# Optimization experiments

Hardware: AMD Instinct MI355X
Metric: run time of the kernel (lower is better)

The kernel has to match this reference:

```python
import jax, jax.numpy as jnp
import numpy as np

NUM_BLOCKS = 3
NUM_CLUSTER = [16, 32, 64]


def _conv(x, w, b):
    # 1x1 conv2d + ReLU (BN folded to identity, eval-mode default stats): x [B,d,N], w [o,d], b [o]
    return jax.nn.relu(jnp.einsum('bdn,od->bon', x, w) + b[None, :, None])


def _segment_pool(feat, idx, nc):
    # Faithful single-pass version of pooling_block: per-cluster max over N,
    # rebroadcast to every node of that cluster. feat [B,d,N], idx [B,N] int.
    B, d, N = feat.shape
    seg = (idx + jnp.arange(B, dtype=idx.dtype)[:, None] * nc).reshape(-1)  # [B*N]
    flat = feat.transpose(0, 2, 1).reshape(B * N, d)
    mx = jax.ops.segment_max(flat, seg, num_segments=B * nc)  # [B*nc, d]
    return mx[seg].reshape(B, N, d).transpose(0, 2, 1)  # [B,d,N]


def setup_inputs() -> dict:
    key = jax.random.key(0)
    ks = jax.random.split(key, 16)
    B, N, K = 8, 16384, 28
    s = 0.05
    f32 = jnp.float32
    return {
        'x': jax.random.normal(ks[0], (B, N, K), f32),
        'clusters': jax.random.randint(ks[1], (NUM_BLOCKS, B, N), 0, min(NUM_CLUSTER), dtype=jnp.int32),
        'w_in': jax.random.normal(ks[2], (256, K), f32) * s,
        'b_in': jnp.zeros((256,), f32),
        'w1': jax.random.normal(ks[3], (NUM_BLOCKS, 64, 256), f32) * s,
        'b1': jnp.zeros((NUM_BLOCKS, 64), f32),
        'w2': jax.random.normal(ks[4], (NUM_BLOCKS, 128, 64), f32) * s,
        'b2': jnp.zeros((NUM_BLOCKS, 128), f32),
        'w3': jax.random.normal(ks[5], (NUM_BLOCKS, 128, 128), f32) * s,
        'b3': jnp.zeros((NUM_BLOCKS, 128), f32),
        'w_out1': jax.random.normal(ks[6], (128, 256), f32) * s,
        'b_out1': jnp.zeros((128,), f32),
        'w_out2': jax.random.normal(ks[7], (128, 128), f32) * s,
        'b_out2': jnp.zeros((128,), f32),
    }


def reference(x, clusters, w_in, b_in, w1, b1, w2, b2, w3, b3, w_out1, b_out1, w_out2, b_out2):
    # mlp_in: conv2d kernel [1,28] contracts the feature width -> [B,256,N]
    f = jax.nn.relu(jnp.einsum('bnk,ok->bon', x, w_in) + b_in[None, :, None])
    for i in range(NUM_BLOCKS):
        f = _conv(f, w1[i], b1[i])          # [B,64,N]
        f = _conv(f, w2[i], b2[i])          # [B,128,N]
        pool = _segment_pool(f, clusters[i], NUM_CLUSTER[i])  # [B,128,N]
        f3 = _conv(f, w3[i], b3[i])         # [B,128,N]
        f = jnp.concatenate([f3, pool], axis=1)  # [B,256,N]
    o1 = _conv(f, w_out1, b_out1)           # [B,128,N]
    o2 = _conv(o1, w_out2, b_out2)          # [B,128,N]
    out_max = o2.max(axis=2)                # global max pool over N
    B, d = out_max.shape
    return out_max.reshape(B, d, 1, 1)
```

## Files before the change

kernel.cpp:

```cpp
#include <hip/hip_runtime.h>


typedef __attribute__((ext_vector_type(8))) short bf16x8;
typedef __attribute__((ext_vector_type(4))) float f32x4;
typedef __attribute__((ext_vector_type(4))) unsigned u32x4;
typedef __attribute__((ext_vector_type(4))) float f32x4v;

#define MFMA16(a, b, c) __builtin_amdgcn_mfma_f32_16x16x32_bf16((a), (b), (c), 0, 0, 0)

#define TPB 512
#define PT 64
#define NPTS 131072
#define NC 16
#define TILES 4
#define NBLK 512

#define FSB 136
#define ASB 72
#define XSB 40

#define U_F256 0
#define U_W1_0 16
#define U_W2_0 48
#define U_W3_0 64
#define U_W1_1 96
#define U_W2_1 112
#define U_W3_1 128
#define U_W1_2 160
#define U_W2_2 176
#define U_W3_2 192
#define U_O1   224
#define U_O2   256
#define N_UNITS 288

__device__ __forceinline__ f32x4 relu4(f32x4 a) {
#pragma unroll
  for (int r = 0; r < 4; ++r) a[r] = fmaxf(a[r], 0.f);
  return a;
}

__device__ __forceinline__ bf16x8 afrag(const short* plane, int stride, int mt, int ks) {
  const int lane = threadIdx.x & 63;
  return *reinterpret_cast<const bf16x8*>(
      plane + (mt * 16 + (lane & 15)) * stride + ks * 32 + (lane >> 4) * 8);
}

__device__ __forceinline__ void bfrag(const unsigned* __restrict__ arena, int unit,
                                      bf16x8& h, bf16x8& l) {
  const bf16x8* p = reinterpret_cast<const bf16x8*>(
      arena + ((size_t)unit * 64 + (threadIdx.x & 63)) * 8);
  h = p[0];
  l = p[1];
}

__device__ __forceinline__ void store_planes(short* hp, short* lp, int stride,
                                             int mt, int n, f32x4 d) {
  const int m0 = mt * 16 + ((threadIdx.x & 63) >> 4) * 4;
#pragma unroll
  for (int r = 0; r < 4; ++r) {
    unsigned uv = __float_as_uint(d[r]);
    unsigned hm = uv & 0xFFFF0000u;
    float lo = d[r] - __uint_as_float(hm);
    hp[(m0 + r) * stride + n] = (short)(hm >> 16);
    lp[(m0 + r) * stride + n] = (short)(__float_as_uint(lo) >> 16);
  }
}

__device__ __forceinline__ void stage_f3(const unsigned* __restrict__ f3g, int tile0,
                                         short* Fhi, short* Flo, int tid) {
  const u32x4* src = reinterpret_cast<const u32x4*>(f3g + (size_t)tile0 * 128);
#pragma unroll
  for (int rr = 0; rr < 4; ++rr) {
    const int idx = rr * TPB + tid;
    const u32x4 p = __builtin_nontemporal_load(src + idx);
    const int pt = idx >> 5, c4 = (idx & 31) * 4;
    uint2 hd, ld;
    hd.x = (p.y & 0xFFFF0000u) | (p.x >> 16);
    hd.y = (p.w & 0xFFFF0000u) | (p.z >> 16);
    ld.x = (p.y << 16) | (p.x & 0xFFFFu);
    ld.y = (p.w << 16) | (p.z & 0xFFFFu);
    *reinterpret_cast<uint2*>(&Fhi[pt * FSB + c4]) = hd;
    *reinterpret_cast<uint2*>(&Flo[pt * FSB + c4]) = ld;
  }
}

__device__ __forceinline__ void write_f3(unsigned* __restrict__ f3g, int tile0,
                                         const short* Fhi, const short* Flo, int tid) {
  u32x4* dst = reinterpret_cast<u32x4*>(f3g + (size_t)tile0 * 128);
#pragma unroll
  for (int rr = 0; rr < 4; ++rr) {
    const int idx = rr * TPB + tid;
    const int pt = idx >> 5, c4 = (idx & 31) * 4;
    const uint2 hd = *reinterpret_cast<const uint2*>(&Fhi[pt * FSB + c4]);
    const uint2 ld = *reinterpret_cast<const uint2*>(&Flo[pt * FSB + c4]);
    u32x4 p;
    p.x = (hd.x << 16) | (ld.x & 0xFFFFu);
    p.y = (hd.x & 0xFFFF0000u) | (ld.x >> 16);
    p.z = (hd.y << 16) | (ld.y & 0xFFFFu);
    p.w = (hd.y & 0xFFFF0000u) | (ld.y >> 16);
    __builtin_nontemporal_store(p, dst + idx);
  }
}

__global__ void __launch_bounds__(64) prep_frags(
    const float* __restrict__ w_in, const float* __restrict__ w1,
    const float* __restrict__ w2, const float* __restrict__ w3,
    const float* __restrict__ wo1, const float* __restrict__ wo2,
    unsigned* __restrict__ arena) {
  const int unit = blockIdx.x;
  const int lane = threadIdx.x;
  const float* W; int KS, Klog, rs, u;
  if (unit < U_W1_0)      { W = w_in;                   u = unit - U_F256; KS = 1; Klog = 28;  rs = 28;  }
  else if (unit < U_W2_0) { W = w1;                     u = unit - U_W1_0; KS = 8; Klog = 256; rs = 256; }
  else if (unit < U_W3_0) { W = w2;                     u = unit - U_W2_0; KS = 2; Klog = 64;  rs = 64;  }
  else if (unit < U_W1_1) { W = w3;                     u = unit - U_W3_0; KS = 4; Klog = 128; rs = 128; }
  else if (unit < U_W2_1) { W = w1 + 64 * 256;          u = unit - U_W1_1; KS = 4; Klog = 128; rs = 256; }
  else if (unit < U_W3_1) { W = w2 + 128 * 64;          u = unit - U_W2_1; KS = 2; Klog = 64;  rs = 64;  }
  else if (unit < U_W1_2) { W = w3 + 128 * 128;         u = unit - U_W3_1; KS = 4; Klog = 128; rs = 128; }
  else if (unit < U_W2_2) { W = w1 + 2 * 64 * 256;      u = unit - U_W1_2; KS = 4; Klog = 128; rs = 256; }
  else if (unit < U_W3_2) { W = w2 + 2 * 128 * 64;      u = unit - U_W2_2; KS = 2; Klog = 64;  rs = 64;  }
  else if (unit < U_O1)   { W = w3 + 2 * 128 * 128;     u = unit - U_W3_2; KS = 4; Klog = 128; rs = 128; }
  else if (unit < U_O2)   { W = wo1;                    u = unit - U_O1;   KS = 4; Klog = 128; rs = 256; }
  else                    { W = wo2;                    u = unit - U_O2;   KS = 4; Klog = 128; rs = 128; }
  const int nt = u / KS, ks = u % KS;
  const int n = nt * 16 + (lane & 15);
  const int k0 = ks * 32 + (lane >> 4) * 8;
  unsigned hiD[4], loD[4];
#pragma unroll
  for (int d = 0; d < 4; ++d) {
    unsigned hu[2], lu[2];
#pragma unroll
    for (int e = 0; e < 2; ++e) {
      const int k = k0 + d * 2 + e;
      float v = (k < Klog) ? W[(size_t)n * rs + k] : 0.f;
      unsigned uv = __float_as_uint(v);
      unsigned hm = uv & 0xFFFF0000u;
      float lo = v - __uint_as_float(hm);
      hu[e] = hm >> 16;
      lu[e] = __float_as_uint(lo) >> 16;
    }
    hiD[d] = hu[0] | (hu[1] << 16);
    loD[d] = lu[0] | (lu[1] << 16);
  }
  unsigned* dst = arena + ((size_t)unit * 64 + lane) * 8;
  *reinterpret_cast<uint4*>(dst)     = make_uint4(hiD[0], hiD[1], hiD[2], hiD[3]);
  *reinterpret_cast<uint4*>(dst + 4) = make_uint4(loD[0], loD[1], loD[2], loD[3]);
}

template<int O>
__global__ void __launch_bounds__(1024) pool_reduce_kern(
    const unsigned* __restrict__ part, const float* __restrict__ W,
    const float* __restrict__ bias, float* __restrict__ poolc_g) {
  __shared__ float pfL[2048];
  __shared__ float Wl[O * 129];
  const int tid = threadIdx.x;
  const int b = blockIdx.x;
  for (int i = tid; i < 2048; i += 1024) pfL[i] = __uint_as_float(part[b * 2048 + i]);
  for (int i = tid; i < O * 128; i += 1024) {
    const int o = i >> 7, k = i & 127;
    Wl[o * 129 + k] = W[o * 256 + 128 + k];
  }
  __syncthreads();
  constexpr int SH = (O == 64) ? 6 : 7;
  for (int e = tid; e < O * 16; e += 1024) {
    const int o = e & (O - 1);
    const int cl = e >> SH;
    float s = bias[o];
    const float* wr = &Wl[o * 129];
    const float* pr = &pfL[cl];
#pragma unroll 4
    for (int k = 0; k < 128; ++k) s = fmaf(wr[k], pr[k * 16], s);
    poolc_g[(size_t)b * (O * 16) + o * 16 + cl] = s;
  }
}

__global__ void __launch_bounds__(TPB, 4) k0_kern(
    const float* __restrict__ x, const int* __restrict__ cls,
    const float* __restrict__ b_in, const float* __restrict__ b1,
    const float* __restrict__ b2, const float* __restrict__ b3,
    const unsigned* __restrict__ arena,
    unsigned* __restrict__ f3g, unsigned* __restrict__ part0) {
  __shared__ short Fhi[PT * FSB], Flo[PT * FSB];
  __shared__ short XA[PT * ASB * 2];
  __shared__ unsigned pool_s[128 * NC];
  short* Xhi = XA;  short* Xlo = XA + PT * XSB;
  short* Ahi = XA;  short* Alo = XA + PT * ASB;
  const int tid = threadIdx.x;
  const int lane = tid & 63, w = tid >> 6, l15 = lane & 15, quad = lane >> 4;
  const int b = blockIdx.x >> 6;
  const int Nt1 = w & 3, mh = w >> 2;
  for (int i = tid; i < 128 * NC; i += TPB) pool_s[i] = 0u;

  float biH[2];
#pragma unroll
  for (int c = 0; c < 2; ++c) biH[c] = b_in[c * 128 + w * 16 + l15];
  const float b1H = b1[Nt1 * 16 + l15];
  const float b2H = b2[w * 16 + l15];
  const float b3H = b3[w * 16 + l15];
  const int n1 = Nt1 * 16 + l15;
  const int n2 = w * 16 + l15;
  const int xpt = (tid < 448) ? tid / 7 : 0;
  const int xc4 = (tid < 448) ? (tid - xpt * 7) * 4 : 0;

  for (int t = 0; t < TILES; ++t) {
    const int tile0 = (blockIdx.x * TILES + t) * PT;
    if (tid < 448) {
      const f32x4v v = __builtin_nontemporal_load(
          reinterpret_cast<const f32x4v*>(x + (size_t)(tile0 + xpt) * 28 + xc4));
      unsigned h0 = __float_as_uint(v.x) & 0xFFFF0000u, h1 = __float_as_uint(v.y) & 0xFFFF0000u;
      unsigned h2 = __float_as_uint(v.z) & 0xFFFF0000u, h3 = __float_as_uint(v.w) & 0xFFFF0000u;
      uint2 hd, ld;
      hd.x = (h0 >> 16) | h1;
      hd.y = (h2 >> 16) | h3;
      ld.x = (__float_as_uint(v.x - __uint_as_float(h0)) >> 16) |
             (__float_as_uint(v.y - __uint_as_float(h1)) & 0xFFFF0000u);
      ld.y = (__float_as_uint(v.z - __uint_as_float(h2)) >> 16) |
             (__float_as_uint(v.w - __uint_as_float(h3)) & 0xFFFF0000u);
      *reinterpret_cast<uint2*>(&Xhi[xpt * XSB + xc4]) = hd;
      *reinterpret_cast<uint2*>(&Xlo[xpt * XSB + xc4]) = ld;
    } else {
      const int p = tid - 448;
      *reinterpret_cast<uint2*>(&Xhi[p * XSB + 28]) = make_uint2(0u, 0u);
      *reinterpret_cast<uint2*>(&Xlo[p * XSB + 28]) = make_uint2(0u, 0u);
    }
    int clP[4][4];
#pragma unroll
    for (int Mt = 0; Mt < 4; ++Mt) {
      int4 v = *reinterpret_cast<const int4*>(cls + tile0 + Mt * 16 + quad * 4);
      clP[Mt][0] = v.x; clP[Mt][1] = v.y; clP[Mt][2] = v.z; clP[Mt][3] = v.w;
    }
    __syncthreads();
    f32x4 a1[2];
#pragma unroll
    for (int m = 0; m < 2; ++m) a1[m] = {b1H, b1H, b1H, b1H};
#pragma unroll 1
    for (int c = 0; c < 2; ++c) {
      f32x4 f6[4];
#pragma unroll
      for (int Mt = 0; Mt < 4; ++Mt) f6[Mt] = {biH[c], biH[c], biH[c], biH[c]};
      {
        bf16x8 bh, bl;
        bfrag(arena, U_F256 + c * 8 + w, bh, bl);
#pragma unroll
        for (int Mt = 0; Mt < 4; ++Mt) {
          const bf16x8 xah = afrag(Xhi, XSB, Mt, 0), xal = afrag(Xlo, XSB, Mt, 0);
          f6[Mt] = MFMA16(xal, bh, MFMA16(xah, bl, MFMA16(xah, bh, f6[Mt])));
        }
      }
#pragma unroll
      for (int Mt = 0; Mt < 4; ++Mt)
        store_planes(Fhi, Flo, FSB, Mt, n2, relu4(f6[Mt]));
      __syncthreads();
#pragma unroll
      for (int ks = 0; ks < 4; ++ks) {
        bf16x8 bh, bl;
        bfrag(arena, U_W1_0 + Nt1 * 8 + c * 4 + ks, bh, bl);
#pragma unroll
        for (int m = 0; m < 2; ++m) {
          const bf16x8 ah = afrag(Fhi, FSB, mh * 2 + m, ks), al = afrag(Flo, FSB, mh * 2 + m, ks);
          a1[m] = MFMA16(al, bh, MFMA16(ah, bl, MFMA16(ah, bh, a1[m])));
        }
      }
      if (c == 1) {
#pragma unroll
        for (int m = 0; m < 2; ++m)
          store_planes(Ahi, Alo, ASB, mh * 2 + m, n1, relu4(a1[m]));
      }
      __syncthreads();
    }
    f32x4 f2[4];
#pragma unroll
    for (int Mt = 0; Mt < 4; ++Mt) f2[Mt] = {b2H, b2H, b2H, b2H};
#pragma unroll
    for (int ks = 0; ks < 2; ++ks) {
      bf16x8 bh, bl;
      bfrag(arena, U_W2_0 + w * 2 + ks, bh, bl);
#pragma unroll
      for (int Mt = 0; Mt < 4; ++Mt) {
        const bf16x8 ah = afrag(Ahi, ASB, Mt, ks), al = afrag(Alo, ASB, Mt, ks);
        f2[Mt] = MFMA16(al, bh, MFMA16(ah, bl, MFMA16(ah, bh, f2[Mt])));
      }
    }
#pragma unroll
    for (int Mt = 0; Mt < 4; ++Mt) {
      f32x4 d = relu4(f2[Mt]);
#pragma unroll
      for (int r = 0; r < 4; ++r)
        atomicMax(&pool_s[n2 * NC + clP[Mt][r]], __float_as_uint(d[r]));
      store_planes(Fhi, Flo, FSB, Mt, n2, d);
    }
    __syncthreads();
    f32x4 f3a[4];
#pragma unroll
    for (int Mt = 0; Mt < 4; ++Mt) f3a[Mt] = {b3H, b3H, b3H, b3H};
#pragma unroll
    for (int ks = 0; ks < 4; ++ks) {
      bf16x8 bh, bl;
      bfrag(arena, U_W3_0 + w * 4 + ks, bh, bl);
#pragma unroll
      for (int Mt = 0; Mt < 4; ++Mt) {
        const bf16x8 ah = afrag(Fhi, FSB, Mt, ks), al = afrag(Flo, FSB, Mt, ks);
        f3a[Mt] = MFMA16(al, bh, MFMA16(ah, bl, MFMA16(ah, bh, f3a[Mt])));
      }
    }
    __syncthreads();
#pragma unroll
    for (int Mt = 0; Mt < 4; ++Mt)
      store_planes(Fhi, Flo, FSB, Mt, n2, relu4(f3a[Mt]));
    __syncthreads();
    write_f3(f3g, tile0, Fhi, Flo, tid);
  }
  for (int i = tid; i < 128 * NC; i += TPB)
    atomicMax(&part0[(size_t)b * 2048 + i], pool_s[i]);
}

__global__ void __launch_bounds__(TPB, 4) kmid_kern(
    unsigned* __restrict__ f3g, const unsigned* __restrict__ arena,
    const float* __restrict__ poolc_g, unsigned* __restrict__ part_cur,
    const int* __restrict__ clg, const int* __restrict__ clp,
    const float* __restrict__ b2s, const float* __restrict__ b3s,
    int uW1, int uW2, int uW3) {
  __shared__ short Fhi[PT * FSB], Flo[PT * FSB];
  __shared__ short Ahi[PT * ASB], Alo[PT * ASB];
  __shared__ unsigned pool_s[128 * NC];
  const int tid = threadIdx.x;
  const int lane = tid & 63, w = tid >> 6, l15 = lane & 15, quad = lane >> 4;
  const int b = blockIdx.x >> 6;
  const int Nt1 = w & 3, mh = w >> 2;
  for (int i = tid; i < 128 * NC; i += TPB) pool_s[i] = 0u;
  const float b2H = b2s[w * 16 + l15];
  const float b3H = b3s[w * 16 + l15];
  const int n1 = Nt1 * 16 + l15;
  const int n2 = w * 16 + l15;

  for (int t = 0; t < TILES; ++t) {
    const int tile0 = (blockIdx.x * TILES + t) * PT;
    stage_f3(f3g, tile0, Fhi, Flo, tid);
    int clG[2][4], clP[4][4];
#pragma unroll
    for (int m = 0; m < 2; ++m) {
      int4 v = *reinterpret_cast<const int4*>(clg + tile0 + (mh * 2 + m) * 16 + quad * 4);
      clG[m][0] = v.x; clG[m][1] = v.y; clG[m][2] = v.z; clG[m][3] = v.w;
    }
#pragma unroll
    for (int Mt = 0; Mt < 4; ++Mt) {
      int4 v = *reinterpret_cast<const int4*>(clp + tile0 + Mt * 16 + quad * 4);
      clP[Mt][0] = v.x; clP[Mt][1] = v.y; clP[Mt][2] = v.z; clP[Mt][3] = v.w;
    }
    __syncthreads();
    f32x4 a1[2];
#pragma unroll
    for (int m = 0; m < 2; ++m)
#pragma unroll
      for (int r = 0; r < 4; ++r)
        a1[m][r] = poolc_g[(size_t)b * 1024 + n1 * 16 + clG[m][r]];
#pragma unroll
    for (int ks = 0; ks < 4; ++ks) {
      bf16x8 bh, bl;
      bfrag(arena, uW1 + Nt1 * 4 + ks, bh, bl);
#pragma unroll
      for (int m = 0; m < 2; ++m) {
        const bf16x8 ah = afrag(Fhi, FSB, mh * 2 + m, ks), al = afrag(Flo, FSB, mh * 2 + m, ks);
        a1[m] = MFMA16(al, bh, MFMA16(ah, bl, MFMA16(ah, bh, a1[m])));
      }
    }
#pragma unroll
    for (int m = 0; m < 2; ++m)
      store_planes(Ahi, Alo, ASB, mh * 2 + m, n1, relu4(a1[m]));
    __syncthreads();
    f32x4 f2[4];
#pragma unroll
    for (int Mt = 0; Mt < 4; ++Mt) f2[Mt] = {b2H, b2H, b2H, b2H};
#pragma unroll
    for (int ks = 0; ks < 2; ++ks) {
      bf16x8 bh, bl;
      bfrag(arena, uW2 + w * 2 + ks, bh, bl);
#pragma unroll
      for (int Mt = 0; Mt < 4; ++Mt) {
        const bf16x8 ah = afrag(Ahi, ASB, Mt, ks), al = afrag(Alo, ASB, Mt, ks);
        f2[Mt] = MFMA16(al, bh, MFMA16(ah, bl, MFMA16(ah, bh, f2[Mt])));
      }
    }
#pragma unroll
    for (int Mt = 0; Mt < 4; ++Mt) {
      f32x4 d = relu4(f2[Mt]);
#pragma unroll
      for (int r = 0; r < 4; ++r)
        atomicMax(&pool_s[n2 * NC + clP[Mt][r]], __float_as_uint(d[r]));
      store_planes(Fhi, Flo, FSB, Mt, n2, d);
    }
    __syncthreads();
    f32x4 f3a[4];
#pragma unroll
    for (int Mt = 0; Mt < 4; ++Mt) f3a[Mt] = {b3H, b3H, b3H, b3H};
#pragma unroll
    for (int ks = 0; ks < 4; ++ks) {
      bf16x8 bh, bl;
      bfrag(arena, uW3 + w * 4 + ks, bh, bl);
#pragma unroll
      for (int Mt = 0; Mt < 4; ++Mt) {
        const bf16x8 ah = afrag(Fhi, FSB, Mt, ks), al = afrag(Flo, FSB, Mt, ks);
        f3a[Mt] = MFMA16(al, bh, MFMA16(ah, bl, MFMA16(ah, bh, f3a[Mt])));
      }
    }
    __syncthreads();
#pragma unroll
    for (int Mt = 0; Mt < 4; ++Mt)
      store_planes(Fhi, Flo, FSB, Mt, n2, relu4(f3a[Mt]));
    __syncthreads();
    write_f3(f3g, tile0, Fhi, Flo, tid);
    __syncthreads();
  }
  for (int i = tid; i < 128 * NC; i += TPB)
    atomicMax(&part_cur[(size_t)b * 2048 + i], pool_s[i]);
}

__global__ void __launch_bounds__(TPB, 4) k3_kern(
    const unsigned* __restrict__ f3g, const unsigned* __restrict__ arena,
    const float* __restrict__ poolco_g, const int* __restrict__ clg,
    const float* __restrict__ bo2, unsigned* __restrict__ out) {
  __shared__ short Fhi[PT * FSB], Flo[PT * FSB];
  const int tid = threadIdx.x;
  const int lane = tid & 63, w = tid >> 6, l15 = lane & 15, quad = lane >> 4;
  const int b = blockIdx.x >> 6;
  const float bo2H = bo2[w * 16 + l15];
  const int n2 = w * 16 + l15;
  float omax = 0.f;

  for (int t = 0; t < TILES; ++t) {
    const int tile0 = (blockIdx.x * TILES + t) * PT;
    stage_f3(f3g, tile0, Fhi, Flo, tid);
    int clA[4][4];
#pragma unroll
    for (int Mt = 0; Mt < 4; ++Mt) {
      int4 v = *reinterpret_cast<const int4*>(clg + tile0 + Mt * 16 + quad * 4);
      clA[Mt][0] = v.x; clA[Mt][1] = v.y; clA[Mt][2] = v.z; clA[Mt][3] = v.w;
    }
    __syncthreads();
    f32x4 o1a[4];
#pragma unroll
    for (int Mt = 0; Mt < 4; ++Mt)
#pragma unroll
      for (int r = 0; r < 4; ++r)
        o1a[Mt][r] = poolco_g[(size_t)b * 2048 + n2 * 16 + clA[Mt][r]];
#pragma unroll
    for (int ks = 0; ks < 4; ++ks) {
      bf16x8 bh, bl;
      bfrag(arena, U_O1 + w * 4 + ks, bh, bl);
#pragma unroll
      for (int Mt = 0; Mt < 4; ++Mt) {
        const bf16x8 ah = afrag(Fhi, FSB, Mt, ks), al = afrag(Flo, FSB, Mt, ks);
        o1a[Mt] = MFMA16(al, bh, MFMA16(ah, bl, MFMA16(ah, bh, o1a[Mt])));
      }
    }
    __syncthreads();
#pragma unroll
    for (int Mt = 0; Mt < 4; ++Mt)
      store_planes(Fhi, Flo, FSB, Mt, n2, relu4(o1a[Mt]));
    __syncthreads();
    f32x4 o2a[4];
#pragma unroll
    for (int Mt = 0; Mt < 4; ++Mt) o2a[Mt] = {bo2H, bo2H, bo2H, bo2H};
#pragma unroll
    for (int ks = 0; ks < 4; ++ks) {
      bf16x8 bh, bl;
      bfrag(arena, U_O2 + w * 4 + ks, bh, bl);
#pragma unroll
      for (int Mt = 0; Mt < 4; ++Mt) {
        const bf16x8 ah = afrag(Fhi, FSB, Mt, ks), al = afrag(Flo, FSB, Mt, ks);
        o2a[Mt] = MFMA16(al, bh, MFMA16(ah, bl, MFMA16(ah, bh, o2a[Mt])));
      }
    }
#pragma unroll
    for (int Mt = 0; Mt < 4; ++Mt) {
      f32x4 d = relu4(o2a[Mt]);
      omax = fmaxf(omax, fmaxf(fmaxf(d[0], d[1]), fmaxf(d[2], d[3])));
    }
    __syncthreads();
  }
  omax = fmaxf(omax, __shfl_xor(omax, 16));
  omax = fmaxf(omax, __shfl_xor(omax, 32));
  if (lane < 16)
    atomicMax(&out[b * 128 + w * 16 + lane], __float_as_uint(omax));
}

extern "C" void kernel_launch(void* const* d_in, const int* in_sizes, int n_in,
                              void* d_out, int out_size, void* d_ws, size_t ws_size,
                              hipStream_t stream) {
  const float* x    = (const float*)d_in[0];
  const int*   cls  = (const int*)d_in[1];
  const float* w_in = (const float*)d_in[2];
  const float* b_in = (const float*)d_in[3];
  const float* w1   = (const float*)d_in[4];
  const float* b1   = (const float*)d_in[5];
  const float* w2   = (const float*)d_in[6];
  const float* b2   = (const float*)d_in[7];
  const float* w3   = (const float*)d_in[8];
  const float* b3   = (const float*)d_in[9];
  const float* wo1  = (const float*)d_in[10];
  const float* bo1  = (const float*)d_in[11];
  const float* wo2  = (const float*)d_in[12];
  const float* bo2  = (const float*)d_in[13];

  char* ws = (char*)d_ws;
  unsigned* f3g = (unsigned*)ws;
  unsigned* part0 = (unsigned*)(ws + ((size_t)64 << 20));
  unsigned* part1 = part0 + 8 * 2048;
  unsigned* part2 = part1 + 8 * 2048;
  float* poolc1 = (float*)(part2 + 8 * 2048);
  float* poolc2 = poolc1 + 8 * 1024;
  float* poolco = poolc2 + 8 * 1024;
  unsigned* arena = (unsigned*)(poolco + 8 * 2048);

  hipMemsetAsync(d_out, 0, 1024 * sizeof(float), stream);
  hipMemsetAsync(part0, 0, 3 * 8 * 2048 * sizeof(unsigned), stream);

  prep_frags<<<N_UNITS, 64, 0, stream>>>(w_in, w1, w2, w3, wo1, wo2, arena);
  k0_kern<<<NBLK, TPB, 0, stream>>>(x, cls, b_in, b1, b2, b3, arena, f3g, part0);
  pool_reduce_kern<64><<<8, 1024, 0, stream>>>(part0, w1 + (size_t)64 * 256, b1 + 64, poolc1);
  kmid_kern<<<NBLK, TPB, 0, stream>>>(f3g, arena, poolc1, part1, cls, cls + NPTS,
                                      b2 + 128, b3 + 128, U_W1_1, U_W2_1, U_W3_1);
  pool_reduce_kern<64><<<8, 1024, 0, stream>>>(part1, w1 + (size_t)2 * 64 * 256, b1 + 128, poolc2);
  kmid_kern<<<NBLK, TPB, 0, stream>>>(f3g, arena, poolc2, part2, cls + NPTS, cls + 2 * NPTS,
                                      b2 + 256, b3 + 256, U_W1_2, U_W2_2, U_W3_2);
  pool_reduce_kern<128><<<8, 1024, 0, stream>>>(part2, wo1, bo1, poolco);
  k3_kern<<<NBLK, TPB, 0, stream>>>(f3g, arena, poolco, cls + 2 * NPTS, bo2, (unsigned*)d_out);
}
```

Measured before the change: 413.6 us.

## Fuse all stages into one cooperative kernel keeping features in registers

Replaces the chain of seven per-stage launches with a single cooperative kernel that uses grid-wide syncs between stages. Each workgroup keeps its packed 128-channel feature tiles in registers across blocks instead of writing them to and re-reading them from global memory. The small pool-reduction matmul is spread across 64 workgroups rather than 8. This removes launch gaps and the global round trips of the feature map, but adds six grid barriers, higher register pressure (64 u32 per thread of carried state), and depends on all 512 workgroups being co-resident. Falls back to the old multi-kernel path if the cooperative launch is unavailable.

```diff
diff --git a/kernel.cpp b/kernel.cpp
--- a/kernel.cpp
+++ b/kernel.cpp
@@ -1,5 +1,8 @@
 #include <hip/hip_runtime.h>
-
+#include <hip/hip_cooperative_groups.h>
+
+
+namespace cg = cooperative_groups;
 
 typedef __attribute__((ext_vector_type(8))) short bf16x8;
 typedef __attribute__((ext_vector_type(4))) float f32x4;
@@ -33,6 +36,16 @@
 #define U_O2   256
 #define N_UNITS 288
 
+__device__ __forceinline__ float agent_ldf(const float* p) {
+  return __hip_atomic_load(p, __ATOMIC_RELAXED, __HIP_MEMORY_SCOPE_AGENT);
+}
+__device__ __forceinline__ unsigned agent_ldu(const unsigned* p) {
+  return __hip_atomic_load(p, __ATOMIC_RELAXED, __HIP_MEMORY_SCOPE_AGENT);
+}
+__device__ __forceinline__ void agent_stf(float* p, float v) {
+  __hip_atomic_store(p, v, __ATOMIC_RELAXED, __HIP_MEMORY_SCOPE_AGENT);
+}
+
 __device__ __forceinline__ f32x4 relu4(f32x4 a) {
 #pragma unroll
   for (int r = 0; r < 4; ++r) a[r] = fmaxf(a[r], 0.f);
@@ -99,6 +112,40 @@
     p.z = (hd.y << 16) | (ld.y & 0xFFFFu);
     p.w = (hd.y & 0xFFFF0000u) | (ld.y >> 16);
     __builtin_nontemporal_store(p, dst + idx);
+  }
+}
+
+__device__ __forceinline__ void unpack_cf(const u32x4 (&c)[4], short* Fhi, short* Flo,
+                                          int tid) {
+#pragma unroll
+  for (int rr = 0; rr < 4; ++rr) {
+    const int idx = rr * TPB + tid;
+    const int pt = idx >> 5, c4 = (idx & 31) * 4;
+    const u32x4 p = c[rr];
+    uint2 hd, ld;
+    hd.x = (p.y & 0xFFFF0000u) | (p.x >> 16);
+    hd.y = (p.w & 0xFFFF0000u) | (p.z >> 16);
+    ld.x = (p.y << 16) | (p.x & 0xFFFFu);
+    ld.y = (p.w << 16) | (p.z & 0xFFFFu);
+    *reinterpret_cast<uint2*>(&Fhi[pt * FSB + c4]) = hd;
+    *reinterpret_cast<uint2*>(&Flo[pt * FSB + c4]) = ld;
+  }
+}
+
+__device__ __forceinline__ void pack_cf(u32x4 (&c)[4], const short* Fhi, const short* Flo,
+                                        int tid) {
+#pragma unroll
+  for (int rr = 0; rr < 4; ++rr) {
+    const int idx = rr * TPB + tid;
+    const int pt = idx >> 5, c4 = (idx & 31) * 4;
+    const uint2 hd = *reinterpret_cast<const uint2*>(&Fhi[pt * FSB + c4]);
+    const uint2 ld = *reinterpret_cast<const uint2*>(&Flo[pt * FSB + c4]);
+    u32x4 p;
+    p.x = (hd.x << 16) | (ld.x & 0xFFFFu);
+    p.y = (hd.x & 0xFFFF0000u) | (ld.x >> 16);
+    p.z = (hd.y << 16) | (ld.y & 0xFFFFu);
+    p.w = (hd.y & 0xFFFF0000u) | (ld.y >> 16);
+    c[rr] = p;
   }
 }
 
@@ -147,6 +194,7 @@
   *reinterpret_cast<uint4*>(dst + 4) = make_uint4(loD[0], loD[1], loD[2], loD[3]);
 }
 
+
 template<int O>
 __global__ void __launch_bounds__(1024) pool_reduce_kern(
     const unsigned* __restrict__ part, const float* __restrict__ W,
@@ -484,6 +532,372 @@
     atomicMax(&out[b * 128 + w * 16 + lane], __float_as_uint(omax));
 }
 
+
+__device__ __forceinline__ void poolc_phase(const unsigned* __restrict__ part,
+                                            const float* __restrict__ W,
+                                            const float* __restrict__ bias,
+                                            float* __restrict__ poolc,
+                                            int O, int tid, int wg) {
+  const int b = wg >> 3, j = wg & 7;
+  const int per = O >> 3;
+  const int njobs = per * 16;
+  if (tid < njobs) {
+    const int o = j * per + (tid >> 4);
+    const int cl = tid & 15;
+    float s = bias[o];
+    const float* wr = W + (size_t)o * 256 + 128;
+    const unsigned* pr = part + b * 2048 + cl;
+#pragma unroll 4
+    for (int k = 0; k < 128; ++k) s = fmaf(wr[k], __uint_as_float(agent_ldu(pr + k * 16)), s);
+    agent_stf(poolc + (size_t)b * (O * 16) + o * 16 + cl, s);
+  }
+}
+
+__device__ __forceinline__ void stage0_body(
+    u32x4 (&cf)[TILES][4],
+    const float* __restrict__ x, const int* __restrict__ cls,
+    const float* __restrict__ b_in, const float* __restrict__ b1,
+    const float* __restrict__ b2, const float* __restrict__ b3,
+    const unsigned* __restrict__ arena, unsigned* __restrict__ part0,
+    short* Fhi, short* Flo, short* XA, unsigned* pool_s,
+    int tid, int wg, int b) {
+  short* Xhi = XA;  short* Xlo = XA + PT * XSB;
+  short* Ahi = XA;  short* Alo = XA + PT * ASB;
+  const int lane = tid & 63, w = tid >> 6, l15 = lane & 15, quad = lane >> 4;
+  const int Nt1 = w & 3, mh = w >> 2;
+  for (int i = tid; i < 128 * NC; i += TPB) pool_s[i] = 0u;
+
+  float biH[2];
+#pragma unroll
+  for (int c = 0; c < 2; ++c) biH[c] = b_in[c * 128 + w * 16 + l15];
+  const float b1H = b1[Nt1 * 16 + l15];
+  const float b2H = b2[w * 16 + l15];
+  const float b3H = b3[w * 16 + l15];
+  const int n1 = Nt1 * 16 + l15;
+  const int n2 = w * 16 + l15;
+  const int xpt = (tid < 448) ? tid / 7 : 0;
+  const int xc4 = (tid < 448) ? (tid - xpt * 7) * 4 : 0;
+
+#pragma unroll
+  for (int t = 0; t < TILES; ++t) {
+    const int tile0 = (wg * TILES + t) * PT;
+    if (tid < 448) {
+      const f32x4v v = __builtin_nontemporal_load(
+          reinterpret_cast<const f32x4v*>(x + (size_t)(tile0 + xpt) * 28 + xc4));
+      unsigned h0 = __float_as_uint(v.x) & 0xFFFF0000u, h1 = __float_as_uint(v.y) & 0xFFFF0000u;
+      unsigned h2 = __float_as_uint(v.z) & 0xFFFF0000u, h3 = __float_as_uint(v.w) & 0xFFFF0000u;
+      uint2 hd, ld;
+      hd.x = (h0 >> 16) | h1;
+      hd.y = (h2 >> 16) | h3;
+      ld.x = (__float_as_uint(v.x - __uint_as_float(h0)) >> 16) |
+             (__float_as_uint(v.y - __uint_as_float(h1)) & 0xFFFF0000u);
+      ld.y = (__float_as_uint(v.z - __uint_as_float(h2)) >> 16) |
+             (__float_as_uint(v.w - __uint_as_float(h3)) & 0xFFFF0000u);
+      *reinterpret_cast<uint2*>(&Xhi[xpt * XSB + xc4]) = hd;
+      *reinterpret_cast<uint2*>(&Xlo[xpt * XSB + xc4]) = ld;
+    } else {
+      const int p = tid - 448;
+      *reinterpret_cast<uint2*>(&Xhi[p * XSB + 28]) = make_uint2(0u, 0u);
+      *reinterpret_cast<uint2*>(&Xlo[p * XSB + 28]) = make_uint2(0u, 0u);
+    }
+    int clP[4][4];
+#pragma unroll
+    for (int Mt = 0; Mt < 4; ++Mt) {
+      int4 v = *reinterpret_cast<const int4*>(cls + tile0 + Mt * 16 + quad * 4);
+      clP[Mt][0] = v.x; clP[Mt][1] = v.y; clP[Mt][2] = v.z; clP[Mt][3] = v.w;
+    }
+    __syncthreads();
+    f32x4 a1[2];
+#pragma unroll
+    for (int m = 0; m < 2; ++m) a1[m] = {b1H, b1H, b1H, b1H};
+#pragma unroll 1
+    for (int c = 0; c < 2; ++c) {
+      f32x4 f6[4];
+#pragma unroll
+      for (int Mt = 0; Mt < 4; ++Mt) f6[Mt] = {biH[c], biH[c], biH[c], biH[c]};
+      {
+        bf16x8 bh, bl;
+        bfrag(arena, U_F256 + c * 8 + w, bh, bl);
+#pragma unroll
+        for (int Mt = 0; Mt < 4; ++Mt) {
+          const bf16x8 xah = afrag(Xhi, XSB, Mt, 0), xal = afrag(Xlo, XSB, Mt, 0);
+          f6[Mt] = MFMA16(xal, bh, MFMA16(xah, bl, MFMA16(xah, bh, f6[Mt])));
+        }
+      }
+#pragma unroll
+      for (int Mt = 0; Mt < 4; ++Mt)
+        store_planes(Fhi, Flo, FSB, Mt, n2, relu4(f6[Mt]));
+      __syncthreads();
+#pragma unroll
+      for (int ks = 0; ks < 4; ++ks) {
+        bf16x8 bh, bl;
+        bfrag(arena, U_W1_0 + Nt1 * 8 + c * 4 + ks, bh, bl);
+#pragma unroll
+        for (int m = 0; m < 2; ++m) {
+          const bf16x8 ah = afrag(Fhi, FSB, mh * 2 + m, ks), al = afrag(Flo, FSB, mh * 2 + m, ks);
+          a1[m] = MFMA16(al, bh, MFMA16(ah, bl, MFMA16(ah, bh, a1[m])));
+        }
+      }
+      if (c == 1) {
+#pragma unroll
+        for (int m = 0; m < 2; ++m)
+          store_planes(Ahi, Alo, ASB, mh * 2 + m, n1, relu4(a1[m]));
+      }
+      __syncthreads();
+    }
+    f32x4 f2[4];
+#pragma unroll
+    for (int Mt = 0; Mt < 4; ++Mt) f2[Mt] = {b2H, b2H, b2H, b2H};
+#pragma unroll
+    for (int ks = 0; ks < 2; ++ks) {
+      bf16x8 bh, bl;
+      bfrag(arena, U_W2_0 + w * 2 + ks, bh, bl);
+#pragma unroll
+      for (int Mt = 0; Mt < 4; ++Mt) {
+        const bf16x8 ah = afrag(Ahi, ASB, Mt, ks), al = afrag(Alo, ASB, Mt, ks);
+        f2[Mt] = MFMA16(al, bh, MFMA16(ah, bl, MFMA16(ah, bh, f2[Mt])));
+      }
+    }
+#pragma unroll
+    for (int Mt = 0; Mt < 4; ++Mt) {
+      f32x4 d = relu4(f2[Mt]);
+#pragma unroll
+      for (int r = 0; r < 4; ++r)
+        atomicMax(&pool_s[n2 * NC + clP[Mt][r]], __float_as_uint(d[r]));
+      store_planes(Fhi, Flo, FSB, Mt, n2, d);
+    }
+    __syncthreads();
+    f32x4 f3a[4];
+#pragma unroll
+    for (int Mt = 0; Mt < 4; ++Mt) f3a[Mt] = {b3H, b3H, b3H, b3H};
+#pragma unroll
+    for (int ks = 0; ks < 4; ++ks) {
+      bf16x8 bh, bl;
+      bfrag(arena, U_W3_0 + w * 4 + ks, bh, bl);
+#pragma unroll
+      for (int Mt = 0; Mt < 4; ++Mt) {
+        const bf16x8 ah = afrag(Fhi, FSB, Mt, ks), al = afrag(Flo, FSB, Mt, ks);
+        f3a[Mt] = MFMA16(al, bh, MFMA16(ah, bl, MFMA16(ah, bh, f3a[Mt])));
+      }
+    }
+    __syncthreads();
+#pragma unroll
+    for (int Mt = 0; Mt < 4; ++Mt)
+      store_planes(Fhi, Flo, FSB, Mt, n2, relu4(f3a[Mt]));
+    __syncthreads();
+    pack_cf(cf[t], Fhi, Flo, tid);
+  }
+  for (int i = tid; i < 128 * NC; i += TPB)
+    atomicMax(&part0[(size_t)b * 2048 + i], pool_s[i]);
+}
+
+__device__ __forceinline__ void mid_body(
+    u32x4 (&cf)[TILES][4], const unsigned* __restrict__ arena,
+    const float* __restrict__ poolc_g, unsigned* __restrict__ part_cur,
+    const int* __restrict__ clg, const int* __restrict__ clp,
+    const float* __restrict__ b2s, const float* __restrict__ b3s,
+    int uW1, int uW2, int uW3,
+    short* Fhi, short* Flo, short* Ahi, short* Alo, unsigned* pool_s,
+    int tid, int wg, int b) {
+  const int lane = tid & 63, w = tid >> 6, l15 = lane & 15, quad = lane >> 4;
+  const int Nt1 = w & 3, mh = w >> 2;
+  for (int i = tid; i < 128 * NC; i += TPB) pool_s[i] = 0u;
+  const float b2H = b2s[w * 16 + l15];
+  const float b3H = b3s[w * 16 + l15];
+  const int n1 = Nt1 * 16 + l15;
+  const int n2 = w * 16 + l15;
+
+#pragma unroll
+  for (int t = 0; t < TILES; ++t) {
+    const int tile0 = (wg * TILES + t) * PT;
+    unpack_cf(cf[t], Fhi, Flo, tid);
+    int clG[2][4], clP[4][4];
+#pragma unroll
+    for (int m = 0; m < 2; ++m) {
+      int4 v = *reinterpret_cast<const int4*>(clg + tile0 + (mh * 2 + m) * 16 + quad * 4);
+      clG[m][0] = v.x; clG[m][1] = v.y; clG[m][2] = v.z; clG[m][3] = v.w;
+    }
+#pragma unroll
+    for (int Mt = 0; Mt < 4; ++Mt) {
+      int4 v = *reinterpret_cast<const int4*>(clp + tile0 + Mt * 16 + quad * 4);
+      clP[Mt][0] = v.x; clP[Mt][1] = v.y; clP[Mt][2] = v.z; clP[Mt][3] = v.w;
+    }
+    __syncthreads();
+    f32x4 a1[2];
+#pragma unroll
+    for (int m = 0; m < 2; ++m)
+#pragma unroll
+      for (int r = 0; r < 4; ++r)
+        a1[m][r] = agent_ldf(poolc_g + (size_t)b * 1024 + n1 * 16 + clG[m][r]);
+#pragma unroll
+    for (int ks = 0; ks < 4; ++ks) {
+      bf16x8 bh, bl;
+      bfrag(arena, uW1 + Nt1 * 4 + ks, bh, bl);
+#pragma unroll
+      for (int m = 0; m < 2; ++m) {
+        const bf16x8 ah = afrag(Fhi, FSB, mh * 2 + m, ks), al = afrag(Flo, FSB, mh * 2 + m, ks);
+        a1[m] = MFMA16(al, bh, MFMA16(ah, bl, MFMA16(ah, bh, a1[m])));
+      }
+    }
+#pragma unroll
+    for (int m = 0; m < 2; ++m)
+      store_planes(Ahi, Alo, ASB, mh * 2 + m, n1, relu4(a1[m]));
+    __syncthreads();
+    f32x4 f2[4];
+#pragma unroll
+    for (int Mt = 0; Mt < 4; ++Mt) f2[Mt] = {b2H, b2H, b2H, b2H};
+#pragma unroll
+    for (int ks = 0; ks < 2; ++ks) {
+      bf16x8 bh, bl;
+      bfrag(arena, uW2 + w * 2 + ks, bh, bl);
+#pragma unroll
+      for (int Mt = 0; Mt < 4; ++Mt) {
+        const bf16x8 ah = afrag(Ahi, ASB, Mt, ks), al = afrag(Alo, ASB, Mt, ks);
+        f2[Mt] = MFMA16(al, bh, MFMA16(ah, bl, MFMA16(ah, bh, f2[Mt])));
+      }
+    }
+#pragma unroll
+    for (int Mt = 0; Mt < 4; ++Mt) {
+      f32x4 d = relu4(f2[Mt]);
+#pragma unroll
+      for (int r = 0; r < 4; ++r)
+        atomicMax(&pool_s[n2 * NC + clP[Mt][r]], __float_as_uint(d[r]));
+      store_planes(Fhi, Flo, FSB, Mt, n2, d);
+    }
+    __syncthreads();
+    f32x4 f3a[4];
+#pragma unroll
+    for (int Mt = 0; Mt < 4; ++Mt) f3a[Mt] = {b3H, b3H, b3H, b3H};
+#pragma unroll
+    for (int ks = 0; ks < 4; ++ks) {
+      bf16x8 bh, bl;
+      bfrag(arena, uW3 + w * 4 + ks, bh, bl);
+#pragma unroll
+      for (int Mt = 0; Mt < 4; ++Mt) {
+        const bf16x8 ah = afrag(Fhi, FSB, Mt, ks), al = afrag(Flo, FSB, Mt, ks);
+        f3a[Mt] = MFMA16(al, bh, MFMA16(ah, bl, MFMA16(ah, bh, f3a[Mt])));
+      }
+    }
+    __syncthreads();
+#pragma unroll
+    for (int Mt = 0; Mt < 4; ++Mt)
+      store_planes(Fhi, Flo, FSB, Mt, n2, relu4(f3a[Mt]));
+    __syncthreads();
+    pack_cf(cf[t], Fhi, Flo, tid);
+    __syncthreads();
+  }
+  for (int i = tid; i < 128 * NC; i += TPB)
+    atomicMax(&part_cur[(size_t)b * 2048 + i], pool_s[i]);
+}
+
+__device__ __forceinline__ void head_body(
+    const u32x4 (&cf)[TILES][4], const unsigned* __restrict__ arena,
+    const float* __restrict__ poolco_g, const int* __restrict__ clg,
+    const float* __restrict__ bo2, unsigned* __restrict__ out,
+    short* Fhi, short* Flo, int tid, int wg, int b) {
+  const int lane = tid & 63, w = tid >> 6, l15 = lane & 15, quad = lane >> 4;
+  const float bo2H = bo2[w * 16 + l15];
+  const int n2 = w * 16 + l15;
+  float omax = 0.f;
+
+#pragma unroll
+  for (int t = 0; t < TILES; ++t) {
+    const int tile0 = (wg * TILES + t) * PT;
+    unpack_cf(cf[t], Fhi, Flo, tid);
+    int clA[4][4];
+#pragma unroll
+    for (int Mt = 0; Mt < 4; ++Mt) {
+      int4 v = *reinterpret_cast<const int4*>(clg + tile0 + Mt * 16 + quad * 4);
+      clA[Mt][0] = v.x; clA[Mt][1] = v.y; clA[Mt][2] = v.z; clA[Mt][3] = v.w;
+    }
+    __syncthreads();
+    f32x4 o1a[4];
+#pragma unroll
+    for (int Mt = 0; Mt < 4; ++Mt)
+#pragma unroll
+      for (int r = 0; r < 4; ++r)
+        o1a[Mt][r] = agent_ldf(poolco_g + (size_t)b * 2048 + n2 * 16 + clA[Mt][r]);
+#pragma unroll
+    for (int ks = 0; ks < 4; ++ks) {
+      bf16x8 bh, bl;
+      bfrag(arena, U_O1 + w * 4 + ks, bh, bl);
+#pragma unroll
+      for (int Mt = 0; Mt < 4; ++Mt) {
+        const bf16x8 ah = afrag(Fhi, FSB, Mt, ks), al = afrag(Flo, FSB, Mt, ks);
+        o1a[Mt] = MFMA16(al, bh, MFMA16(ah, bl, MFMA16(ah, bh, o1a[Mt])));
+      }
+    }
+    __syncthreads();
+#pragma unroll
+    for (int Mt = 0; Mt < 4; ++Mt)
+      store_planes(Fhi, Flo, FSB, Mt, n2, relu4(o1a[Mt]));
+    __syncthreads();
+    f32x4 o2a[4];
+#pragma unroll
+    for (int Mt = 0; Mt < 4; ++Mt) o2a[Mt] = {bo2H, bo2H, bo2H, bo2H};
+#pragma unroll
+    for (int ks = 0; ks < 4; ++ks) {
+      bf16x8 bh, bl;
+      bfrag(arena, U_O2 + w * 4 + ks, bh, bl);
+#pragma unroll
+      for (int Mt = 0; Mt < 4; ++Mt) {
+        const bf16x8 ah = afrag(Fhi, FSB, Mt, ks), al = afrag(Flo, FSB, Mt, ks);
+        o2a[Mt] = MFMA16(al, bh, MFMA16(ah, bl, MFMA16(ah, bh, o2a[Mt])));
+      }
+    }
+#pragma unroll
+    for (int Mt = 0; Mt < 4; ++Mt) {
+      f32x4 d = relu4(o2a[Mt]);
+      omax = fmaxf(omax, fmaxf(fmaxf(d[0], d[1]), fmaxf(d[2], d[3])));
+    }
+    __syncthreads();
+  }
+  omax = fmaxf(omax, __shfl_xor(omax, 16));
+  omax = fmaxf(omax, __shfl_xor(omax, 32));
+  if (lane < 16)
+    atomicMax(&out[b * 128 + w * 16 + lane], __float_as_uint(omax));
+}
+
+struct FusedParams {
+  const float* x; const int* cls;
+  const float* b_in; const float* b1; const float* b2; const float* b3;
+  const float* w1; const float* wo1; const float* bo1; const float* bo2;
+  const unsigned* arena;
+  unsigned* part0; unsigned* part1; unsigned* part2;
+  float* poolc1; float* poolc2; float* poolco;
+  unsigned* out;
+};
+
+__global__ void __launch_bounds__(TPB, 4) fused_kern(FusedParams P) {
+  __shared__ short Fhi[PT * FSB], Flo[PT * FSB];
+  __shared__ short XA[PT * ASB * 2];
+  __shared__ unsigned pool_s[128 * NC];
+  const int tid = threadIdx.x;
+  const int wg = blockIdx.x;
+  const int b = wg >> 6;
+  u32x4 cf[TILES][4];
+
+  stage0_body(cf, P.x, P.cls, P.b_in, P.b1, P.b2, P.b3, P.arena, P.part0,
+              Fhi, Flo, XA, pool_s, tid, wg, b);
+  cg::this_grid().sync();
+  if (wg < 64) poolc_phase(P.part0, P.w1 + 64 * 256, P.b1 + 64, P.poolc1, 64, tid, wg);
+  cg::this_grid().sync();
+  mid_body(cf, P.arena, P.poolc1, P.part1, P.cls, P.cls + NPTS,
+           P.b2 + 128, P.b3 + 128, U_W1_1, U_W2_1, U_W3_1,
+           Fhi, Flo, XA, XA + PT * ASB, pool_s, tid, wg, b);
+  cg::this_grid().sync();
+  if (wg < 64) poolc_phase(P.part1, P.w1 + 2 * 64 * 256, P.b1 + 128, P.poolc2, 64, tid, wg);
+  cg::this_grid().sync();
+  mid_body(cf, P.arena, P.poolc2, P.part2, P.cls + NPTS, P.cls + 2 * NPTS,
+           P.b2 + 256, P.b3 + 256, U_W1_2, U_W2_2, U_W3_2,
+           Fhi, Flo, XA, XA + PT * ASB, pool_s, tid, wg, b);
+  cg::this_grid().sync();
+  if (wg < 64) poolc_phase(P.part2, P.wo1, P.bo1, P.poolco, 128, tid, wg);
+  cg::this_grid().sync();
+  head_body(cf, P.arena, P.poolco, P.cls + 2 * NPTS, P.bo2, P.out,
+            Fhi, Flo, tid, wg, b);
+}
+
 extern "C" void kernel_launch(void* const* d_in, const int* in_sizes, int n_in,
                               void* d_out, int out_size, void* d_ws, size_t ws_size,
                               hipStream_t stream) {
@@ -516,13 +930,41 @@
   hipMemsetAsync(part0, 0, 3 * 8 * 2048 * sizeof(unsigned), stream);
 
   prep_frags<<<N_UNITS, 64, 0, stream>>>(w_in, w1, w2, w3, wo1, wo2, arena);
-  k0_kern<<<NBLK, TPB, 0, stream>>>(x, cls, b_in, b1, b2, b3, arena, f3g, part0);
-  pool_reduce_kern<64><<<8, 1024, 0, stream>>>(part0, w1 + (size_t)64 * 256, b1 + 64, poolc1);
-  kmid_kern<<<NBLK, TPB, 0, stream>>>(f3g, arena, poolc1, part1, cls, cls + NPTS,
-                                      b2 + 128, b3 + 128, U_W1_1, U_W2_1, U_W3_1);
-  pool_reduce_kern<64><<<8, 1024, 0, stream>>>(part1, w1 + (size_t)2 * 64 * 256, b1 + 128, poolc2);
-  kmid_kern<<<NBLK, TPB, 0, stream>>>(f3g, arena, poolc2, part2, cls + NPTS, cls + 2 * NPTS,
-                                      b2 + 256, b3 + 256, U_W1_2, U_W2_2, U_W3_2);
-  pool_reduce_kern<128><<<8, 1024, 0, stream>>>(part2, wo1, bo1, poolco);
-  k3_kern<<<NBLK, TPB, 0, stream>>>(f3g, arena, poolco, cls + 2 * NPTS, bo2, (unsigned*)d_out);
-}
+
+  static int coop_ok = -1;
+  if (coop_ok < 0) {
+    int maxb = 0;
+    hipError_t oe = hipOccupancyMaxActiveBlocksPerMultiprocessor(
+        &maxb, (const void*)fused_kern, TPB, 0);
+    coop_ok = (oe == hipSuccess && maxb >= 2) ? 1 : 0;
+    if (oe != hipSuccess) (void)hipGetLastError();
+  }
+
+  bool fused_done = false;
+  if (coop_ok == 1) {
+    FusedParams P{x, cls, b_in, b1, b2, b3, w1, wo1, bo1, bo2,
+                  arena, part0, part1, part2, poolc1, poolc2, poolco,
+                  (unsigned*)d_out};
+    void* args[] = {&P};
+    hipError_t le = hipLaunchCooperativeKernel((void*)fused_kern, dim3(NBLK),
+                                               dim3(TPB), args, 0, stream);
+    if (le == hipSuccess) {
+      fused_done = true;
+    } else {
+      (void)hipGetLastError();
+      coop_ok = 0;
+    }
+  }
+
+  if (!fused_done) {
+    k0_kern<<<NBLK, TPB, 0, stream>>>(x, cls, b_in, b1, b2, b3, arena, f3g, part0);
+    pool_reduce_kern<64><<<8, 1024, 0, stream>>>(part0, w1 + (size_t)64 * 256, b1 + 64, poolc1);
+    kmid_kern<<<NBLK, TPB, 0, stream>>>(f3g, arena, poolc1, part1, cls, cls + NPTS,
+                                        b2 + 128, b3 + 128, U_W1_1, U_W2_1, U_W3_1);
+    pool_reduce_kern<64><<<8, 1024, 0, stream>>>(part1, w1 + (size_t)2 * 64 * 256, b1 + 128, poolc2);
+    kmid_kern<<<NBLK, TPB, 0, stream>>>(f3g, arena, poolc2, part2, cls + NPTS, cls + 2 * NPTS,
+                                        b2 + 256, b3 + 256, U_W1_2, U_W2_2, U_W3_2);
+    pool_reduce_kern<128><<<8, 1024, 0, stream>>>(part2, wo1, bo1, poolco);
+    k3_kern<<<NBLK, TPB, 0, stream>>>(f3g, arena, poolco, cls + 2 * NPTS, bo2, (unsigned*)d_out);
+  }
+}
```

Result: no change. 416.2 us (+0.6%).

## Fuse pool-reduce into consumer kernels and prefetch next tile into registers

Applied to the files above, without the earlier changes.

Removes the three small pool_reduce launches. Each kmid and k3 block now recomputes the per-cluster pool contribution table (W·poolmax) into shared memory at kernel start from the partial max buffer. It also software-prefetches the next tile of x or f3 into registers after the sync, so global loads overlap with MFMA compute. This trades launch overhead and serial tiny kernels for redundant per-block recomputation (512 blocks each doing a 128-deep dot for every table entry, with weights read from global) and extra register pressure.

```diff
diff --git a/kernel.cpp b/kernel.cpp
--- a/kernel.cpp
+++ b/kernel.cpp
@@ -66,14 +66,21 @@
   }
 }
 
-__device__ __forceinline__ void stage_f3(const unsigned* __restrict__ f3g, int tile0,
-                                         short* Fhi, short* Flo, int tid) {
+__device__ __forceinline__ void pf_load(const unsigned* __restrict__ f3g, int tile0,
+                                        int tid, u32x4 (&pf)[4]) {
   const u32x4* src = reinterpret_cast<const u32x4*>(f3g + (size_t)tile0 * 128);
+#pragma unroll
+  for (int rr = 0; rr < 4; ++rr)
+    pf[rr] = __builtin_nontemporal_load(src + rr * TPB + tid);
+}
+
+__device__ __forceinline__ void pf_stage(const u32x4 (&pf)[4], short* Fhi, short* Flo,
+                                         int tid) {
 #pragma unroll
   for (int rr = 0; rr < 4; ++rr) {
     const int idx = rr * TPB + tid;
-    const u32x4 p = __builtin_nontemporal_load(src + idx);
     const int pt = idx >> 5, c4 = (idx & 31) * 4;
+    const u32x4 p = pf[rr];
     uint2 hd, ld;
     hd.x = (p.y & 0xFFFF0000u) | (p.x >> 16);
     hd.y = (p.w & 0xFFFF0000u) | (p.z >> 16);
@@ -147,33 +154,6 @@
   *reinterpret_cast<uint4*>(dst + 4) = make_uint4(loD[0], loD[1], loD[2], loD[3]);
 }
 
-template<int O>
-__global__ void __launch_bounds__(1024) pool_reduce_kern(
-    const unsigned* __restrict__ part, const float* __restrict__ W,
-    const float* __restrict__ bias, float* __restrict__ poolc_g) {
-  __shared__ float pfL[2048];
-  __shared__ float Wl[O * 129];
-  const int tid = threadIdx.x;
-  const int b = blockIdx.x;
-  for (int i = tid; i < 2048; i += 1024) pfL[i] = __uint_as_float(part[b * 2048 + i]);
-  for (int i = tid; i < O * 128; i += 1024) {
-    const int o = i >> 7, k = i & 127;
-    Wl[o * 129 + k] = W[o * 256 + 128 + k];
-  }
-  __syncthreads();
-  constexpr int SH = (O == 64) ? 6 : 7;
-  for (int e = tid; e < O * 16; e += 1024) {
-    const int o = e & (O - 1);
-    const int cl = e >> SH;
-    float s = bias[o];
-    const float* wr = &Wl[o * 129];
-    const float* pr = &pfL[cl];
-#pragma unroll 4
-    for (int k = 0; k < 128; ++k) s = fmaf(wr[k], pr[k * 16], s);
-    poolc_g[(size_t)b * (O * 16) + o * 16 + cl] = s;
-  }
-}
-
 __global__ void __launch_bounds__(TPB, 4) k0_kern(
     const float* __restrict__ x, const int* __restrict__ cls,
     const float* __restrict__ b_in, const float* __restrict__ b1,
@@ -202,11 +182,15 @@
   const int xpt = (tid < 448) ? tid / 7 : 0;
   const int xc4 = (tid < 448) ? (tid - xpt * 7) * 4 : 0;
 
+  f32x4v xv = {0.f, 0.f, 0.f, 0.f};
+  if (tid < 448)
+    xv = __builtin_nontemporal_load(reinterpret_cast<const f32x4v*>(
+        x + (size_t)(blockIdx.x * TILES * PT + xpt) * 28 + xc4));
+
   for (int t = 0; t < TILES; ++t) {
     const int tile0 = (blockIdx.x * TILES + t) * PT;
     if (tid < 448) {
-      const f32x4v v = __builtin_nontemporal_load(
-          reinterpret_cast<const f32x4v*>(x + (size_t)(tile0 + xpt) * 28 + xc4));
+      const f32x4v v = xv;
       unsigned h0 = __float_as_uint(v.x) & 0xFFFF0000u, h1 = __float_as_uint(v.y) & 0xFFFF0000u;
       unsigned h2 = __float_as_uint(v.z) & 0xFFFF0000u, h3 = __float_as_uint(v.w) & 0xFFFF0000u;
       uint2 hd, ld;
@@ -230,6 +214,9 @@
       clP[Mt][0] = v.x; clP[Mt][1] = v.y; clP[Mt][2] = v.z; clP[Mt][3] = v.w;
     }
     __syncthreads();
+    if (t + 1 < TILES && tid < 448)
+      xv = __builtin_nontemporal_load(reinterpret_cast<const f32x4v*>(
+          x + (size_t)(tile0 + PT + xpt) * 28 + xc4));
     f32x4 a1[2];
 #pragma unroll
     for (int m = 0; m < 2; ++m) a1[m] = {b1H, b1H, b1H, b1H};
@@ -316,26 +303,48 @@
 
 __global__ void __launch_bounds__(TPB, 4) kmid_kern(
     unsigned* __restrict__ f3g, const unsigned* __restrict__ arena,
-    const float* __restrict__ poolc_g, unsigned* __restrict__ part_cur,
+    const unsigned* __restrict__ part_prev, const float* __restrict__ w1p,
+    const float* __restrict__ b1p, unsigned* __restrict__ part_cur,
     const int* __restrict__ clg, const int* __restrict__ clp,
     const float* __restrict__ b2s, const float* __restrict__ b3s,
     int uW1, int uW2, int uW3) {
   __shared__ short Fhi[PT * FSB], Flo[PT * FSB];
   __shared__ short Ahi[PT * ASB], Alo[PT * ASB];
   __shared__ unsigned pool_s[128 * NC];
+  __shared__ float pltab[1024];
   const int tid = threadIdx.x;
   const int lane = tid & 63, w = tid >> 6, l15 = lane & 15, quad = lane >> 4;
   const int b = blockIdx.x >> 6;
   const int Nt1 = w & 3, mh = w >> 2;
-  for (int i = tid; i < 128 * NC; i += TPB) pool_s[i] = 0u;
   const float b2H = b2s[w * 16 + l15];
   const float b3H = b3s[w * 16 + l15];
   const int n1 = Nt1 * 16 + l15;
   const int n2 = w * 16 + l15;
 
+  u32x4 pf[4];
+  pf_load(f3g, blockIdx.x * TILES * PT, tid, pf);
+
+  {
+    float* tmp = reinterpret_cast<float*>(Fhi);
+    for (int i = tid; i < 2048; i += TPB)
+      tmp[i] = __uint_as_float(part_prev[(size_t)b * 2048 + i]);
+    for (int i = tid; i < 128 * NC; i += TPB) pool_s[i] = 0u;
+    __syncthreads();
+    for (int e = tid; e < 1024; e += TPB) {
+      const int o = e >> 4, cl = e & 15;
+      float s = b1p[o];
+      const float* wr = w1p + (size_t)o * 256 + 128;
+      const float* pr = tmp + cl;
+#pragma unroll 4
+      for (int k = 0; k < 128; ++k) s = fmaf(wr[k], pr[k * 16], s);
+      pltab[o * 16 + cl] = s;
+    }
+    __syncthreads();
+  }
+
   for (int t = 0; t < TILES; ++t) {
     const int tile0 = (blockIdx.x * TILES + t) * PT;
-    stage_f3(f3g, tile0, Fhi, Flo, tid);
+    pf_stage(pf, Fhi, Flo, tid);
     int clG[2][4], clP[4][4];
 #pragma unroll
     for (int m = 0; m < 2; ++m) {
@@ -348,12 +357,13 @@
       clP[Mt][0] = v.x; clP[Mt][1] = v.y; clP[Mt][2] = v.z; clP[Mt][3] = v.w;
     }
     __syncthreads();
+    if (t + 1 < TILES) pf_load(f3g, tile0 + PT, tid, pf);
     f32x4 a1[2];
 #pragma unroll
     for (int m = 0; m < 2; ++m)
 #pragma unroll
       for (int r = 0; r < 4; ++r)
-        a1[m][r] = poolc_g[(size_t)b * 1024 + n1 * 16 + clG[m][r]];
+        a1[m][r] = pltab[n1 * 16 + clG[m][r]];
 #pragma unroll
     for (int ks = 0; ks < 4; ++ks) {
       bf16x8 bh, bl;
@@ -417,9 +427,11 @@
 
 __global__ void __launch_bounds__(TPB, 4) k3_kern(
     const unsigned* __restrict__ f3g, const unsigned* __restrict__ arena,
-    const float* __restrict__ poolco_g, const int* __restrict__ clg,
+    const unsigned* __restrict__ part_prev, const float* __restrict__ wo1,
+    const float* __restrict__ bo1, const int* __restrict__ clg,
     const float* __restrict__ bo2, unsigned* __restrict__ out) {
   __shared__ short Fhi[PT * FSB], Flo[PT * FSB];
+  __shared__ float ptab[2048];
   const int tid = threadIdx.x;
   const int lane = tid & 63, w = tid >> 6, l15 = lane & 15, quad = lane >> 4;
   const int b = blockIdx.x >> 6;
@@ -427,9 +439,29 @@
   const int n2 = w * 16 + l15;
   float omax = 0.f;
 
+  u32x4 pf[4];
+  pf_load(f3g, blockIdx.x * TILES * PT, tid, pf);
+
+  {
+    float* tmp = reinterpret_cast<float*>(Fhi);
+    for (int i = tid; i < 2048; i += TPB)
+      tmp[i] = __uint_as_float(part_prev[(size_t)b * 2048 + i]);
+    __syncthreads();
+    for (int e = tid; e < 2048; e += TPB) {
+      const int o = e >> 4, cl = e & 15;
+      float s = bo1[o];
+      const float* wr = wo1 + (size_t)o * 256 + 128;
+      const float* pr = tmp + cl;
+#pragma unroll 4
+      for (int k = 0; k < 128; ++k) s = fmaf(wr[k], pr[k * 16], s);
+      ptab[o * 16 + cl] = s;
+    }
+    __syncthreads();
+  }
+
   for (int t = 0; t < TILES; ++t) {
     const int tile0 = (blockIdx.x * TILES + t) * PT;
-    stage_f3(f3g, tile0, Fhi, Flo, tid);
+    pf_stage(pf, Fhi, Flo, tid);
     int clA[4][4];
 #pragma unroll
     for (int Mt = 0; Mt < 4; ++Mt) {
@@ -437,12 +469,13 @@
       clA[Mt][0] = v.x; clA[Mt][1] = v.y; clA[Mt][2] = v.z; clA[Mt][3] = v.w;
     }
     __syncthreads();
+    if (t + 1 < TILES) pf_load(f3g, tile0 + PT, tid, pf);
     f32x4 o1a[4];
 #pragma unroll
     for (int Mt = 0; Mt < 4; ++Mt)
 #pragma unroll
       for (int r = 0; r < 4; ++r)
-        o1a[Mt][r] = poolco_g[(size_t)b * 2048 + n2 * 16 + clA[Mt][r]];
+        o1a[Mt][r] = ptab[n2 * 16 + clA[Mt][r]];
 #pragma unroll
     for (int ks = 0; ks < 4; ++ks) {
       bf16x8 bh, bl;
@@ -507,22 +540,19 @@
   unsigned* part0 = (unsigned*)(ws + ((size_t)64 << 20));
   unsigned* part1 = part0 + 8 * 2048;
   unsigned* part2 = part1 + 8 * 2048;
-  float* poolc1 = (float*)(part2 + 8 * 2048);
-  float* poolc2 = poolc1 + 8 * 1024;
-  float* poolco = poolc2 + 8 * 1024;
-  unsigned* arena = (unsigned*)(poolco + 8 * 2048);
+  unsigned* arena = part2 + 8 * 2048;
 
   hipMemsetAsync(d_out, 0, 1024 * sizeof(float), stream);
   hipMemsetAsync(part0, 0, 3 * 8 * 2048 * sizeof(unsigned), stream);
 
   prep_frags<<<N_UNITS, 64, 0, stream>>>(w_in, w1, w2, w3, wo1, wo2, arena);
   k0_kern<<<NBLK, TPB, 0, stream>>>(x, cls, b_in, b1, b2, b3, arena, f3g, part0);
-  pool_reduce_kern<64><<<8, 1024, 0, stream>>>(part0, w1 + (size_t)64 * 256, b1 + 64, poolc1);
-  kmid_kern<<<NBLK, TPB, 0, stream>>>(f3g, arena, poolc1, part1, cls, cls + NPTS,
+  kmid_kern<<<NBLK, TPB, 0, stream>>>(f3g, arena, part0, w1 + (size_t)64 * 256,
+                                      b1 + 64, part1, cls, cls + NPTS,
                                       b2 + 128, b3 + 128, U_W1_1, U_W2_1, U_W3_1);
-  pool_reduce_kern<64><<<8, 1024, 0, stream>>>(part1, w1 + (size_t)2 * 64 * 256, b1 + 128, poolc2);
-  kmid_kern<<<NBLK, TPB, 0, stream>>>(f3g, arena, poolc2, part2, cls + NPTS, cls + 2 * NPTS,
+  kmid_kern<<<NBLK, TPB, 0, stream>>>(f3g, arena, part1, w1 + (size_t)2 * 64 * 256,
+                                      b1 + 128, part2, cls + NPTS, cls + 2 * NPTS,
                                       b2 + 256, b3 + 256, U_W1_2, U_W2_2, U_W3_2);
-  pool_reduce_kern<128><<<8, 1024, 0, stream>>>(part2, wo1, bo1, poolco);
-  k3_kern<<<NBLK, TPB, 0, stream>>>(f3g, arena, poolco, cls + 2 * NPTS, bo2, (unsigned*)d_out);
-}
+  k3_kern<<<NBLK, TPB, 0, stream>>>(f3g, arena, part2, wo1, bo1,
+                                    cls + 2 * NPTS, bo2, (unsigned*)d_out);
+}
```

Measured after the change: 434.7 us. 5.1% more time.
